# Performance work log

Measured on AMD Instinct MI355X. Metric: run time of the kernel, lower is better.

The kernel has to match this reference:

```python
import jax, jax.numpy as jnp
import numpy as np

N, F, DE = 768, 64, 32
H0, H1, H2, OUT = 64, 64, 128, 1  # hidden_dim=[64,64,128], output_dim=1


def _mlp(x, Wa, ba, Wb, bb):
    # two Dense layers with relu, as in the repo's MLP
    h = jax.nn.relu(x @ Wa + ba)
    return jax.nn.relu(h @ Wb + bb)


def _edge_conv_e(A, x, e, Wa, ba, Wb, bb):
    # EdgeConvE: per-edge message MLP([x_i, x_j - x_i, e_ij]) aggregated
    # over neighbors j weighted by the (binary) adjacency.
    n = x.shape[0]
    xi = jnp.broadcast_to(x[:, None, :], (n, n, x.shape[1]))  # [N,N,F]
    xj = jnp.broadcast_to(x[None, :, :], (n, n, x.shape[1]))  # [N,N,F]
    feat = jnp.concatenate([xi, xj - xi, e], axis=-1)         # [N,N,2F+De]
    m = _mlp(feat, Wa, ba, Wb, bb)                            # [N,N,H]
    return jnp.einsum('ij,ijh->ih', A, m)                     # scatter-sum over j


def setup_inputs() -> dict:
    key = jax.random.key(0)
    ks = jax.random.split(key, 16)
    adj = (jax.random.uniform(ks[0], (N, N)) < 0.05).astype(jnp.float32)
    x = jax.random.normal(ks[1], (N, F), dtype=jnp.float32)
    e = jax.random.normal(ks[2], (N, N, DE), dtype=jnp.float32)
    s = 0.05
    d_in1 = 2 * F + DE          # 160
    d_in2 = 2 * H0 + DE         # 160
    return {
        'ajacency': adj,
        'node_features': x,
        'edge_attributes': e,
        'W1a': jax.random.normal(ks[3], (d_in1, H0)) * s, 'b1a': jnp.zeros((H0,)),
        'W1b': jax.random.normal(ks[4], (H0, H0)) * s,    'b1b': jnp.zeros((H0,)),
        'W2a': jax.random.normal(ks[5], (d_in2, H1)) * s, 'b2a': jnp.zeros((H1,)),
        'W2b': jax.random.normal(ks[6], (H1, H0)) * s,    'b2b': jnp.zeros((H0,)),
        'W3': jax.random.normal(ks[7], (H0, H2)) * s,     'b3': jnp.zeros((H2,)),
        'W4': jax.random.normal(ks[8], (H2, OUT)) * s,    'b4': jnp.zeros((OUT,)),
    }


def reference(ajacency, node_features, edge_attributes,
              W1a, b1a, W1b, b1b, W2a, b2a, W2b, b2b, W3, b3, W4, b4):
    x = _edge_conv_e(ajacency, node_features, edge_attributes, W1a, b1a, W1b, b1b)
    x = _edge_conv_e(ajacency, x, edge_attributes, W2a, b2a, W2b, b2b)
    x = jax.nn.relu(x @ W3 + b3)
    return jax.nn.sigmoid(x @ W4 + b4)  # [N, OUT]
```

## Files before the change

### kernel.cpp

```cpp
#include <hip/hip_runtime.h>
#include <math.h>


#define NN 768
#define FF 64
#define DE 32
#define HH 64
#define CAP 128
#define SH1S 72

using bf16x8 = __attribute__((ext_vector_type(8))) short;
using f32x4  = __attribute__((ext_vector_type(4))) float;

__device__ __forceinline__ short f2b(float f) {
  unsigned u = __float_as_uint(f);
  return (short)((u + 0x7fffu + ((u >> 16) & 1u)) >> 16);
}
__device__ __forceinline__ float b2f(unsigned short u) {
  return __uint_as_float(((unsigned)u) << 16);
}

__device__ __forceinline__ void phaseB(
    const short* sh1b, const short* __restrict__ Wbp,
    const float* __restrict__ bb, float* xrow, int c, int lane, int wv)
{
  if (c > 0) {
    const int nt = (c + 15) >> 4;
    const int q = lane >> 4, n = lane & 15;
    bf16x8 b0 = *(const bf16x8*)(Wbp + (((wv * 2 + 0) * 4 + q) * 16 + n) * 8);
    bf16x8 b1 = *(const bf16x8*)(Wbp + (((wv * 2 + 1) * 4 + q) * 16 + n) * 8);
    const float bias = bb[wv * 16 + n];
    float s = 0.0f;
    for (int rt = 0; rt < nt; ++rt) {
      const short* sa = sh1b + (rt * 16 + n) * SH1S + q * 8;
      bf16x8 a0 = *(const bf16x8*)(sa);
      bf16x8 a1 = *(const bf16x8*)(sa + 32);
      f32x4 acc = {0.f, 0.f, 0.f, 0.f};
      acc = __builtin_amdgcn_mfma_f32_16x16x32_bf16(a0, b0, acc, 0, 0, 0);
      acc = __builtin_amdgcn_mfma_f32_16x16x32_bf16(a1, b1, acc, 0, 0, 0);
#pragma unroll
      for (int reg = 0; reg < 4; ++reg) {
        const int row = rt * 16 + q * 4 + reg;
        const float v = fmaxf(acc[reg] + bias, 0.0f);
        s += (row < c) ? v : 0.0f;
      }
    }
    s += __shfl_down(s, 32);
    s += __shfl_down(s, 16);
    if (lane < 16) xrow[wv * 16 + lane] = s;
  } else {
    if (lane < 16) xrow[wv * 16 + lane] = 0.0f;
  }
}

__global__ __launch_bounds__(256) void scan_kernel(
    const float* __restrict__ A, const float* __restrict__ x,
    const float* __restrict__ W, const float* __restrict__ bias,
    const float* __restrict__ Wb1, const float* __restrict__ Wb2,
    int* __restrict__ cnt, int* __restrict__ jl,
    float* __restrict__ U, float* __restrict__ V,
    short* __restrict__ Wbp1, short* __restrict__ Wbp2)
{
  const int i = blockIdx.x;
  const int tid = threadIdx.x;
  __shared__ int s_cnt;
  __shared__ int s_j[CAP];
  __shared__ float sx[64];
  __shared__ float su[4][64], sv[4][64];

  if (tid == 0) s_cnt = 0;
  __syncthreads();
  if (tid < 64) sx[tid] = x[i * 64 + tid];
  if (tid < NN / 4) {
    float4 a = ((const float4*)(A + i * NN))[tid];
    if (a.x != 0.0f) { int p = atomicAdd(&s_cnt, 1); if (p < CAP) s_j[p] = tid * 4 + 0; }
    if (a.y != 0.0f) { int p = atomicAdd(&s_cnt, 1); if (p < CAP) s_j[p] = tid * 4 + 1; }
    if (a.z != 0.0f) { int p = atomicAdd(&s_cnt, 1); if (p < CAP) s_j[p] = tid * 4 + 2; }
    if (a.w != 0.0f) { int p = atomicAdd(&s_cnt, 1); if (p < CAP) s_j[p] = tid * 4 + 3; }
  }

  if (i < 2) {
    const float* src = (i == 0) ? Wb1 : Wb2;
    short* dst = (i == 0) ? Wbp1 : Wbp2;
    for (int L = tid; L < 4096; L += 256) {
      const int j = L & 7, n = (L >> 3) & 15, quad = (L >> 7) & 3;
      const int kb = (L >> 9) & 1, ct = L >> 10;
      dst[L] = f2b(src[(kb * 32 + quad * 8 + j) * 64 + ct * 16 + n]);
    }
  }
  __syncthreads();
  const int c = min(s_cnt, CAP);

  const int c64 = tid & 63, sg = tid >> 6;
  {
    float u = 0.0f, v = 0.0f;
#pragma unroll
    for (int t = 0; t < 16; ++t) {
      const int d = sg * 16 + t;
      const float xv = sx[d];
      const float wxi = W[d * 64 + c64];
      const float wxj = W[(64 + d) * 64 + c64];
      u = fmaf(xv, wxi - wxj, u);
      v = fmaf(xv, wxj, v);
    }
    su[sg][c64] = u; sv[sg][c64] = v;
  }
  __syncthreads();

  if (tid < 64) {
    U[i * 64 + tid] = su[0][tid] + su[1][tid] + su[2][tid] + su[3][tid] + bias[tid];
    V[i * 64 + tid] = sv[0][tid] + sv[1][tid] + sv[2][tid] + sv[3][tid];
  }
  if (tid == 0) cnt[i] = c;
  for (int t = tid; t < c; t += 256) jl[(i << 7) + t] = s_j[t];
}

__global__ __launch_bounds__(256) void conv1uv2_kernel(
    const int* __restrict__ cnt, const int* __restrict__ jl,
    const float* __restrict__ e,
    const float* __restrict__ U1, const float* __restrict__ V1,
    const float* __restrict__ We1, const float* __restrict__ We2,
    const short* __restrict__ Wbp1, const float* __restrict__ b1b,
    const float* __restrict__ W2a, const float* __restrict__ b2a,
    float* __restrict__ U2, float* __restrict__ V2,
    unsigned short* __restrict__ ew2b)
{
  const int i = blockIdx.x;
  const int tid = threadIdx.x, lane = tid & 63, wv = tid >> 6;
  __shared__ __align__(16) float es[CAP][DE];
  __shared__ __align__(16) short sh1b[CAP * SH1S];
  __shared__ int s_j[CAP];
  __shared__ float xrow[64];
  __shared__ float su[4][64], sv[4][64];

  const int c = cnt[i];
  for (int t = tid; t < c; t += 256) s_j[t] = jl[(i << 7) + t];
  __syncthreads();

  for (int slot = tid >> 3; slot < c; slot += 32) {
    const int j = s_j[slot];
    ((float4*)es[slot])[tid & 7] =
        ((const float4*)(e + ((size_t)i * NN + j) * DE))[tid & 7];
  }

  float w1e[DE], w2e[DE];
#pragma unroll
  for (int d = 0; d < DE; ++d) { w1e[d] = We1[d * HH + lane]; w2e[d] = We2[d * HH + lane]; }
  __syncthreads();

  if (c > 0) {
    const int cpad = ((c + 15) >> 4) << 4;
    const float u_i = U1[(i << 6) + lane];
    for (int slot = wv; slot < cpad; slot += 4) {
      short val = 0;
      if (slot < c) {
        const int j = s_j[slot];
        float h = u_i + V1[(j << 6) + lane];
        float g = 0.0f;
#pragma unroll
        for (int d = 0; d < DE; ++d) {
          const float f = es[slot][d];
          h = fmaf(f, w1e[d], h);
          g = fmaf(f, w2e[d], g);
        }
        val = f2b(fmaxf(h, 0.0f));
        ew2b[((size_t)(i << 7) + slot) * HH + lane] = (unsigned short)f2b(g);
      }
      sh1b[slot * SH1S + lane] = val;
    }
  }
  __syncthreads();

  phaseB(sh1b, Wbp1, b1b, xrow, c, lane, wv);
  __syncthreads();

  const int c64 = tid & 63, qr = tid >> 6;
  {
    float u = 0.0f, v = 0.0f;
#pragma unroll
    for (int t = 0; t < 16; ++t) {
      const int d = qr * 16 + t;
      const float xv = xrow[d];
      const float wxi = W2a[d * 64 + c64];
      const float wxj = W2a[(64 + d) * 64 + c64];
      u = fmaf(xv, wxi - wxj, u);
      v = fmaf(xv, wxj, v);
    }
    su[qr][c64] = u; sv[qr][c64] = v;
  }
  __syncthreads();
  if (tid < 64) {
    U2[i * 64 + tid] = su[0][tid] + su[1][tid] + su[2][tid] + su[3][tid] + b2a[tid];
    V2[i * 64 + tid] = sv[0][tid] + sv[1][tid] + sv[2][tid] + sv[3][tid];
  }
}

__global__ __launch_bounds__(256) void conv2head_kernel(
    const int* __restrict__ cnt, const int* __restrict__ jl,
    const float* __restrict__ U2, const float* __restrict__ V2,
    const unsigned short* __restrict__ ew2b, const short* __restrict__ Wbp2,
    const float* __restrict__ b2b,
    const float* __restrict__ W3, const float* __restrict__ b3,
    const float* __restrict__ W4, const float* __restrict__ b4,
    float* __restrict__ out)
{
  const int i = blockIdx.x;
  const int tid = threadIdx.x, lane = tid & 63, wv = tid >> 6;
  __shared__ __align__(16) short sh1b[CAP * SH1S];
  __shared__ float xrow[64];
  __shared__ float sred[2];

  const int c = cnt[i];
  if (c > 0) {
    const int cpad = ((c + 15) >> 4) << 4;
    const float u_i = U2[(i << 6) + lane];
    for (int slot = wv; slot < cpad; slot += 4) {
      short val = 0;
      if (slot < c) {
        const int j = jl[(i << 7) + slot];
        const float h = u_i + V2[(j << 6) + lane]
                      + b2f(ew2b[((size_t)(i << 7) + slot) * HH + lane]);
        val = f2b(fmaxf(h, 0.0f));
      }
      sh1b[slot * SH1S + lane] = val;
    }
  }
  __syncthreads();

  phaseB(sh1b, Wbp2, b2b, xrow, c, lane, wv);
  __syncthreads();

  if (tid < 128) {
    float p = b3[tid];
#pragma unroll
    for (int cc = 0; cc < 64; ++cc) p = fmaf(xrow[cc], W3[cc * 128 + tid], p);
    p = fmaxf(p, 0.0f);
    float v = p * W4[tid];
    v += __shfl_down(v, 32);
    v += __shfl_down(v, 16);
    v += __shfl_down(v, 8);
    v += __shfl_down(v, 4);
    v += __shfl_down(v, 2);
    v += __shfl_down(v, 1);
    if (lane == 0) sred[wv] = v;
  }
  __syncthreads();
  if (tid == 0) {
    const float z = sred[0] + sred[1] + b4[0];
    out[i] = 1.0f / (1.0f + expf(-z));
  }
}

extern "C" void kernel_launch(void* const* d_in, const int* in_sizes, int n_in,
                              void* d_out, int out_size, void* d_ws, size_t ws_size,
                              hipStream_t stream) {
  const float* A   = (const float*)d_in[0];
  const float* x   = (const float*)d_in[1];
  const float* e   = (const float*)d_in[2];
  const float* W1a = (const float*)d_in[3];
  const float* b1a = (const float*)d_in[4];
  const float* W1b = (const float*)d_in[5];
  const float* b1b = (const float*)d_in[6];
  const float* W2a = (const float*)d_in[7];
  const float* b2a = (const float*)d_in[8];
  const float* W2b = (const float*)d_in[9];
  const float* b2b = (const float*)d_in[10];
  const float* W3  = (const float*)d_in[11];
  const float* b3  = (const float*)d_in[12];
  const float* W4  = (const float*)d_in[13];
  const float* b4  = (const float*)d_in[14];
  float* out = (float*)d_out;

  int*   cnt  = (int*)d_ws;
  int*   jl   = cnt + NN;
  float* U1   = (float*)(jl + NN * CAP);
  float* V1   = U1 + NN * HH;
  float* U2   = V1 + NN * HH;
  float* V2   = U2 + NN * HH;
  unsigned short* ew2b = (unsigned short*)(V2 + NN * HH);
  short* Wbp1 = (short*)(ew2b + (size_t)NN * CAP * HH);
  short* Wbp2 = Wbp1 + 4096;

  scan_kernel<<<NN, 256, 0, stream>>>(A, x, W1a, b1a, W1b, W2b,
                                      cnt, jl, U1, V1, Wbp1, Wbp2);
  conv1uv2_kernel<<<NN, 256, 0, stream>>>(cnt, jl, e, U1, V1,
                                          W1a + 128 * HH, W2a + 128 * HH,
                                          Wbp1, b1b, W2a, b2a, U2, V2, ew2b);
  conv2head_kernel<<<NN, 256, 0, stream>>>(cnt, jl, U2, V2, ew2b, Wbp2, b2b,
                                           W3, b3, W4, b4, out);
}
```

Baseline: 153.0 us.

## Compute edge-attribute projections with bf16 MFMA and drop the ew2b intermediate

Replaces the per-lane scalar FMA loop over edge attributes with a bf16 MFMA against pre-packed edge weights (We1p/We2p), packed once in the scan kernel. The second conv layer now re-reads the sparse edge attributes and recomputes its edge projection instead of storing and reloading a bf16 ew2b buffer in global memory. This trades an extra gather of e in the second kernel for removing the ew2b write/read traffic and the scalar FMA work. It also rounds the edge features to bf16 before the projection, which lowers precision.

```diff
diff --git a/kernel.cpp b/kernel.cpp
--- a/kernel.cpp
+++ b/kernel.cpp
@@ -15,9 +15,6 @@
 __device__ __forceinline__ short f2b(float f) {
   unsigned u = __float_as_uint(f);
   return (short)((u + 0x7fffu + ((u >> 16) & 1u)) >> 16);
-}
-__device__ __forceinline__ float b2f(unsigned short u) {
-  return __uint_as_float(((unsigned)u) << 16);
 }
 
 __device__ __forceinline__ void phaseB(
@@ -53,13 +50,53 @@
   }
 }
 
+__device__ __forceinline__ void phaseA(
+    int i, int c, const int* s_j, const float* __restrict__ e,
+    const float* __restrict__ U, const float* __restrict__ V,
+    const short* __restrict__ Wep, short (*esb)[DE], short* sh1b,
+    int tid, int lane, int wv)
+{
+  for (int slot = tid >> 3; slot < c; slot += 32) {
+    const int j = s_j[slot];
+    float4 f = ((const float4*)(e + ((size_t)i * NN + j) * DE))[tid & 7];
+    short4 s4 = { f2b(f.x), f2b(f.y), f2b(f.z), f2b(f.w) };
+    *(short4*)(&esb[slot][(tid & 7) * 4]) = s4;
+  }
+
+  const int q = lane >> 4, n = lane & 15;
+  const int ch = wv * 16 + n;
+  bf16x8 bwe = *(const bf16x8*)(Wep + ((wv * 4 + q) * 16 + n) * 8);
+  const float u_ch = (c > 0) ? U[(i << 6) + ch] : 0.0f;
+  __syncthreads();
+
+  const int nt = (c + 15) >> 4;
+  for (int rt = 0; rt < nt; ++rt) {
+    bf16x8 a = *(const bf16x8*)(&esb[rt * 16 + n][q * 8]);
+    f32x4 P = {0.f, 0.f, 0.f, 0.f};
+    P = __builtin_amdgcn_mfma_f32_16x16x32_bf16(a, bwe, P, 0, 0, 0);
+#pragma unroll
+    for (int reg = 0; reg < 4; ++reg) {
+      const int slot = rt * 16 + q * 4 + reg;
+      short val = 0;
+      if (slot < c) {
+        const int j = s_j[slot];
+        val = f2b(fmaxf(u_ch + V[(j << 6) + ch] + P[reg], 0.0f));
+      }
+      sh1b[slot * SH1S + ch] = val;
+    }
+  }
+  __syncthreads();
+}
+
 __global__ __launch_bounds__(256) void scan_kernel(
     const float* __restrict__ A, const float* __restrict__ x,
     const float* __restrict__ W, const float* __restrict__ bias,
+    const float* __restrict__ We1, const float* __restrict__ We2,
     const float* __restrict__ Wb1, const float* __restrict__ Wb2,
     int* __restrict__ cnt, int* __restrict__ jl,
     float* __restrict__ U, float* __restrict__ V,
-    short* __restrict__ Wbp1, short* __restrict__ Wbp2)
+    short* __restrict__ Wbp1, short* __restrict__ Wbp2,
+    short* __restrict__ We1p, short* __restrict__ We2p)
 {
   const int i = blockIdx.x;
   const int tid = threadIdx.x;
@@ -80,12 +117,18 @@
   }
 
   if (i < 2) {
-    const float* src = (i == 0) ? Wb1 : Wb2;
-    short* dst = (i == 0) ? Wbp1 : Wbp2;
+    const float* srcb = (i == 0) ? Wb1 : Wb2;
+    short* dstb = (i == 0) ? Wbp1 : Wbp2;
     for (int L = tid; L < 4096; L += 256) {
       const int j = L & 7, n = (L >> 3) & 15, quad = (L >> 7) & 3;
       const int kb = (L >> 9) & 1, ct = L >> 10;
-      dst[L] = f2b(src[(kb * 32 + quad * 8 + j) * 64 + ct * 16 + n]);
+      dstb[L] = f2b(srcb[(kb * 32 + quad * 8 + j) * 64 + ct * 16 + n]);
+    }
+    const float* srce = (i == 0) ? We1 : We2;
+    short* dste = (i == 0) ? We1p : We2p;
+    for (int L = tid; L < 2048; L += 256) {
+      const int j = L & 7, n = (L >> 3) & 15, q = (L >> 7) & 3, ct = L >> 9;
+      dste[L] = f2b(srce[(q * 8 + j) * 64 + ct * 16 + n]);
     }
   }
   __syncthreads();
@@ -119,15 +162,14 @@
     const int* __restrict__ cnt, const int* __restrict__ jl,
     const float* __restrict__ e,
     const float* __restrict__ U1, const float* __restrict__ V1,
-    const float* __restrict__ We1, const float* __restrict__ We2,
-    const short* __restrict__ Wbp1, const float* __restrict__ b1b,
+    const short* __restrict__ We1p, const short* __restrict__ Wbp1,
+    const float* __restrict__ b1b,
     const float* __restrict__ W2a, const float* __restrict__ b2a,
-    float* __restrict__ U2, float* __restrict__ V2,
-    unsigned short* __restrict__ ew2b)
+    float* __restrict__ U2, float* __restrict__ V2)
 {
   const int i = blockIdx.x;
   const int tid = threadIdx.x, lane = tid & 63, wv = tid >> 6;
-  __shared__ __align__(16) float es[CAP][DE];
+  __shared__ __align__(16) short esb[CAP][DE];
   __shared__ __align__(16) short sh1b[CAP * SH1S];
   __shared__ int s_j[CAP];
   __shared__ float xrow[64];
@@ -137,40 +179,7 @@
   for (int t = tid; t < c; t += 256) s_j[t] = jl[(i << 7) + t];
   __syncthreads();
 
-  for (int slot = tid >> 3; slot < c; slot += 32) {
-    const int j = s_j[slot];
-    ((float4*)es[slot])[tid & 7] =
-        ((const float4*)(e + ((size_t)i * NN + j) * DE))[tid & 7];
-  }
-
-  float w1e[DE], w2e[DE];
-#pragma unroll
-  for (int d = 0; d < DE; ++d) { w1e[d] = We1[d * HH + lane]; w2e[d] = We2[d * HH + lane]; }
-  __syncthreads();
-
-  if (c > 0) {
-    const int cpad = ((c + 15) >> 4) << 4;
-    const float u_i = U1[(i << 6) + lane];
-    for (int slot = wv; slot < cpad; slot += 4) {
-      short val = 0;
-      if (slot < c) {
-        const int j = s_j[slot];
-        float h = u_i + V1[(j << 6) + lane];
-        float g = 0.0f;
-#pragma unroll
-        for (int d = 0; d < DE; ++d) {
-          const float f = es[slot][d];
-          h = fmaf(f, w1e[d], h);
-          g = fmaf(f, w2e[d], g);
-        }
-        val = f2b(fmaxf(h, 0.0f));
-        ew2b[((size_t)(i << 7) + slot) * HH + lane] = (unsigned short)f2b(g);
-      }
-      sh1b[slot * SH1S + lane] = val;
-    }
-  }
-  __syncthreads();
-
+  phaseA(i, c, s_j, e, U1, V1, We1p, esb, sh1b, tid, lane, wv);
   phaseB(sh1b, Wbp1, b1b, xrow, c, lane, wv);
   __syncthreads();
 
@@ -197,8 +206,9 @@
 
 __global__ __launch_bounds__(256) void conv2head_kernel(
     const int* __restrict__ cnt, const int* __restrict__ jl,
+    const float* __restrict__ e,
     const float* __restrict__ U2, const float* __restrict__ V2,
-    const unsigned short* __restrict__ ew2b, const short* __restrict__ Wbp2,
+    const short* __restrict__ We2p, const short* __restrict__ Wbp2,
     const float* __restrict__ b2b,
     const float* __restrict__ W3, const float* __restrict__ b3,
     const float* __restrict__ W4, const float* __restrict__ b4,
@@ -206,27 +216,17 @@
 {
   const int i = blockIdx.x;
   const int tid = threadIdx.x, lane = tid & 63, wv = tid >> 6;
+  __shared__ __align__(16) short esb[CAP][DE];
   __shared__ __align__(16) short sh1b[CAP * SH1S];
+  __shared__ int s_j[CAP];
   __shared__ float xrow[64];
   __shared__ float sred[2];
 
   const int c = cnt[i];
-  if (c > 0) {
-    const int cpad = ((c + 15) >> 4) << 4;
-    const float u_i = U2[(i << 6) + lane];
-    for (int slot = wv; slot < cpad; slot += 4) {
-      short val = 0;
-      if (slot < c) {
-        const int j = jl[(i << 7) + slot];
-        const float h = u_i + V2[(j << 6) + lane]
-                      + b2f(ew2b[((size_t)(i << 7) + slot) * HH + lane]);
-        val = f2b(fmaxf(h, 0.0f));
-      }
-      sh1b[slot * SH1S + lane] = val;
-    }
-  }
-  __syncthreads();
-
+  for (int t = tid; t < c; t += 256) s_j[t] = jl[(i << 7) + t];
+  __syncthreads();
+
+  phaseA(i, c, s_j, e, U2, V2, We2p, esb, sh1b, tid, lane, wv);
   phaseB(sh1b, Wbp2, b2b, xrow, c, lane, wv);
   __syncthreads();
 
@@ -277,15 +277,17 @@
   float* V1   = U1 + NN * HH;
   float* U2   = V1 + NN * HH;
   float* V2   = U2 + NN * HH;
-  unsigned short* ew2b = (unsigned short*)(V2 + NN * HH);
-  short* Wbp1 = (short*)(ew2b + (size_t)NN * CAP * HH);
+  short* Wbp1 = (short*)(V2 + NN * HH);
   short* Wbp2 = Wbp1 + 4096;
-
-  scan_kernel<<<NN, 256, 0, stream>>>(A, x, W1a, b1a, W1b, W2b,
-                                      cnt, jl, U1, V1, Wbp1, Wbp2);
-  conv1uv2_kernel<<<NN, 256, 0, stream>>>(cnt, jl, e, U1, V1,
-                                          W1a + 128 * HH, W2a + 128 * HH,
-                                          Wbp1, b1b, W2a, b2a, U2, V2, ew2b);
-  conv2head_kernel<<<NN, 256, 0, stream>>>(cnt, jl, U2, V2, ew2b, Wbp2, b2b,
+  short* We1p = Wbp2 + 4096;
+  short* We2p = We1p + 2048;
+
+  scan_kernel<<<NN, 256, 0, stream>>>(A, x, W1a, b1a,
+                                      W1a + 128 * HH, W2a + 128 * HH,
+                                      W1b, W2b,
+                                      cnt, jl, U1, V1, Wbp1, Wbp2, We1p, We2p);
+  conv1uv2_kernel<<<NN, 256, 0, stream>>>(cnt, jl, e, U1, V1, We1p, Wbp1, b1b,
+                                          W2a, b2a, U2, V2);
+  conv2head_kernel<<<NN, 256, 0, stream>>>(cnt, jl, e, U2, V2, We2p, Wbp2, b2b,
                                            W3, b3, W4, b4, out);
 }
```

After: 149.9 us. 1.02x faster.
